# Kernel tuning notes

Hardware: AMD Instinct MI355X
Metric: run time of the kernel (lower is better)

## Reference

```python
import jax, jax.numpy as jnp
import numpy as np

B, S, H, U = 32, 2048, 1024, 1024


def setup_inputs() -> dict:
    key = jax.random.key(0)
    ks = jax.random.split(key, 5)
    sc = 1.0 / np.sqrt(H)
    return {
        "hidden_t": jax.random.normal(ks[0], (B, H), jnp.float32),
        "hiddens": jax.random.normal(ks[1], (B, S, H), jnp.float32),
        "W1": jax.random.normal(ks[2], (H, U), jnp.float32) * sc,
        "b1": jnp.zeros((U,), jnp.float32),
        "W2": jax.random.normal(ks[3], (H, U), jnp.float32) * sc,
        "b2": jnp.zeros((U,), jnp.float32),
        "V": jax.random.normal(ks[4], (U, 1), jnp.float32) * sc,
        "bV": jnp.zeros((1,), jnp.float32),
    }


def reference(hidden_t, hiddens, W1, b1, W2, b2, V, bV):
    # proj of encoder states: [B,S,U]; proj of decoder state broadcast over time: [B,1,U]
    keys = jnp.einsum("bsh,hu->bsu", hiddens, W1) + b1
    query = (hidden_t @ W2 + b2)[:, None, :]
    score = jnp.tanh(keys + query) @ V + bV            # [B,S,1]
    attention_weights = jax.nn.softmax(score, axis=1)  # softmax over seq axis
    context_vector = jnp.sum(attention_weights * hiddens, axis=1)  # [B,H]
    return context_vector, attention_weights
```

## Files before the change

### kernel.cpp

```cpp
#include <hip/hip_runtime.h>
#include <hip/hip_bf16.h>
#include <cstdint>

#define S_LEN 2048
#define B_SZ  32
#define H_DIM 1024
#define U_DIM 1024

#define BM 128
#define BN 128
#define BK 64

using short8  = __attribute__((ext_vector_type(8))) short;
using floatx4 = __attribute__((ext_vector_type(4))) float;

typedef __attribute__((address_space(3))) void lds_void;
typedef const __attribute__((address_space(1))) void glb_void;
#define GLD16(g, s) __builtin_amdgcn_global_load_lds((glb_void*)(g), (lds_void*)(s), 16, 0, 0)

__device__ __forceinline__ unsigned short f32_to_bf16_rne(float f) {
    unsigned int u = __float_as_uint(f);
    unsigned int r = (u + 0x7fffu + ((u >> 16) & 1u)) >> 16;
    return (unsigned short)r;
}

__global__ __launch_bounds__(256)
void cast_hiddens_kernel(const float* __restrict__ src, unsigned short* __restrict__ dst) {
    const size_t i = ((size_t)blockIdx.x * 256 + threadIdx.x) * 8;
    float4 a = *(const float4*)(src + i);
    float4 b = *(const float4*)(src + i + 4);
    ushort4 lo, hi;
    lo.x = f32_to_bf16_rne(a.x); lo.y = f32_to_bf16_rne(a.y);
    lo.z = f32_to_bf16_rne(a.z); lo.w = f32_to_bf16_rne(a.w);
    hi.x = f32_to_bf16_rne(b.x); hi.y = f32_to_bf16_rne(b.y);
    hi.z = f32_to_bf16_rne(b.z); hi.w = f32_to_bf16_rne(b.w);
    *(ushort4*)(dst + i)     = lo;
    *(ushort4*)(dst + i + 4) = hi;
}

__global__ void transpose_cast_w1(const float* __restrict__ W1,
                                  unsigned short* __restrict__ W1t) {
    __shared__ float tile[32][33];
    const int tx = threadIdx.x, ty = threadIdx.y;
    const int u0 = blockIdx.x * 32, h0 = blockIdx.y * 32;
#pragma unroll
    for (int i = 0; i < 4; ++i)
        tile[ty * 4 + i][tx] = W1[(size_t)(h0 + ty * 4 + i) * U_DIM + u0 + tx];
    __syncthreads();
#pragma unroll
    for (int i = 0; i < 4; ++i)
        W1t[(size_t)(u0 + ty * 4 + i) * H_DIM + h0 + tx] =
            f32_to_bf16_rne(tile[tx][ty * 4 + i]);
}

__global__ void query_kernel(const float* __restrict__ hidden_t,
                             const float* __restrict__ W2,
                             const float* __restrict__ b1,
                             const float* __restrict__ b2,
                             float* __restrict__ query) {
    const int b = blockIdx.y;
    const int u = blockIdx.x * 128 + threadIdx.x;
    const float* ht = hidden_t + b * H_DIM;
    float acc = b1[u] + b2[u];
#pragma unroll 8
    for (int h = 0; h < H_DIM; ++h)
        acc = fmaf(ht[h], W2[(size_t)h * U_DIM + u], acc);
    query[b * U_DIM + u] = acc;
}

__device__ __forceinline__ void score_epilogue(const floatx4 acc[4][4],
                                               const float* __restrict__ qrow,
                                               const float* __restrict__ V,
                                               float* __restrict__ scores,
                                               int m0, int n0, int wr, int wc, int q, int r) {
#pragma unroll
    for (int mt = 0; mt < 4; ++mt) {
#pragma unroll
        for (int reg = 0; reg < 4; ++reg) {
            float sum = 0.f;
#pragma unroll
            for (int nt = 0; nt < 4; ++nt) {
                const int c = n0 + wc * 64 + nt * 16 + r;
                float x = acc[mt][nt][reg] + qrow[c];
                x = fminf(fmaxf(x, -15.f), 15.f);
                float e = __expf(2.f * x);
                float t = (e - 1.f) / (e + 1.f);
                sum = fmaf(t, V[c], sum);
            }
            sum += __shfl_xor(sum, 1);
            sum += __shfl_xor(sum, 2);
            sum += __shfl_xor(sum, 4);
            sum += __shfl_xor(sum, 8);
            if (r == 0)
                atomicAdd(&scores[m0 + wr * 64 + mt * 16 + q * 4 + reg], sum);
        }
    }
}

__global__ __launch_bounds__(256)
void keys_score_v3(const unsigned short* __restrict__ hb,
                   const unsigned short* __restrict__ W1t,
                   const float* __restrict__ query,
                   const float* __restrict__ V,
                   float* __restrict__ scores) {
    __shared__ unsigned short As[BM * BK];
    __shared__ unsigned short Bs[BN * BK];

    const int tid = threadIdx.x;
    const int w = tid >> 6, l = tid & 63;
    const int q = l >> 4, r = l & 15;
    const int wr = w >> 1, wc = w & 1;

    const int bid = blockIdx.x;
    const int col      = (bid >> 3) & 7;
    const int row_band = ((bid >> 6) << 3) | (bid & 7);
    const int m0 = row_band * BM;
    const int n0 = col * BN;

    const int srow   = l >> 3;
    const int schunk = (l & 7) * 8;

    const unsigned short* gA = hb  + ((size_t)(m0 + w * 8 + srow) << 10) + schunk;
    const unsigned short* gB = W1t + ((size_t)(n0 + w * 8 + srow) << 10) + schunk;
    unsigned short* lA = &As[(w * 8) * BK];
    unsigned short* lB = &Bs[(w * 8) * BK];

    floatx4 acc[4][4];
#pragma unroll
    for (int mt = 0; mt < 4; ++mt)
#pragma unroll
        for (int nt = 0; nt < 4; ++nt)
            acc[mt][nt] = (floatx4){0.f, 0.f, 0.f, 0.f};

    for (int kt = 0; kt < H_DIM / BK; ++kt) {
#pragma unroll
        for (int i = 0; i < 4; ++i) {
            GLD16(gA + ((size_t)(i * 32) << 10), lA + i * 32 * BK);
            GLD16(gB + ((size_t)(i * 32) << 10), lB + i * 32 * BK);
        }
        gA += BK; gB += BK;

        __syncthreads();

#pragma unroll
        for (int kh = 0; kh < 2; ++kh) {
            short8 af[4], bfr[4];
#pragma unroll
            for (int mt = 0; mt < 4; ++mt)
                af[mt] = *(const short8*)&As[(wr * 64 + mt * 16 + r) * BK + kh * 32 + q * 8];
#pragma unroll
            for (int nt = 0; nt < 4; ++nt)
                bfr[nt] = *(const short8*)&Bs[(wc * 64 + nt * 16 + r) * BK + kh * 32 + q * 8];
#pragma unroll
            for (int mt = 0; mt < 4; ++mt)
#pragma unroll
                for (int nt = 0; nt < 4; ++nt)
                    acc[mt][nt] = __builtin_amdgcn_mfma_f32_16x16x32_bf16(
                        af[mt], bfr[nt], acc[mt][nt], 0, 0, 0);
        }

        __syncthreads();
    }

    const float* qrow = query + (m0 >> 11) * U_DIM;
    score_epilogue(acc, qrow, V, scores, m0, n0, wr, wc, q, r);
}

__global__ __launch_bounds__(256)
void keys_score_v1(const float* __restrict__ hiddens,
                   const unsigned short* __restrict__ W1t,
                   const float* __restrict__ query,
                   const float* __restrict__ V,
                   float* __restrict__ scores) {
    __shared__ unsigned short As[BM][40];
    __shared__ unsigned short Bs[BN][40];
    const int tid = threadIdx.x;
    const int lane = tid & 63, wave = tid >> 6;
    const int q = lane >> 4, r = lane & 15;
    const int wr = wave >> 1, wc = wave & 1;
    const int m0 = blockIdx.y * BM, n0 = blockIdx.x * BN;
    const int arow = tid >> 3, achunk = tid & 7;
    const int brow = tid >> 2, bchunk = tid & 3;
    floatx4 acc[4][4];
#pragma unroll
    for (int mt = 0; mt < 4; ++mt)
#pragma unroll
        for (int nt = 0; nt < 4; ++nt)
            acc[mt][nt] = (floatx4){0.f, 0.f, 0.f, 0.f};
    for (int kt = 0; kt < H_DIM / 32; ++kt) {
        const float* ag = hiddens + (size_t)(m0 + arow) * H_DIM + kt * 32 + achunk * 4;
#pragma unroll
        for (int i = 0; i < 4; ++i) {
            float4 f = *(const float4*)(ag + (size_t)i * 32 * H_DIM);
            ushort4 h;
            h.x = f32_to_bf16_rne(f.x); h.y = f32_to_bf16_rne(f.y);
            h.z = f32_to_bf16_rne(f.z); h.w = f32_to_bf16_rne(f.w);
            *(ushort4*)&As[arow + i * 32][achunk * 4] = h;
        }
        const unsigned short* bg = W1t + (size_t)(n0 + brow) * H_DIM + kt * 32 + bchunk * 8;
#pragma unroll
        for (int i = 0; i < 2; ++i)
            *(uint4*)&Bs[brow + i * 64][bchunk * 8] = *(const uint4*)(bg + (size_t)i * 64 * H_DIM);
        __syncthreads();
        short8 af[4], bfr[4];
#pragma unroll
        for (int mt = 0; mt < 4; ++mt)
            af[mt] = *(const short8*)&As[wr * 64 + mt * 16 + r][q * 8];
#pragma unroll
        for (int nt = 0; nt < 4; ++nt)
            bfr[nt] = *(const short8*)&Bs[wc * 64 + nt * 16 + r][q * 8];
#pragma unroll
        for (int mt = 0; mt < 4; ++mt)
#pragma unroll
            for (int nt = 0; nt < 4; ++nt)
                acc[mt][nt] = __builtin_amdgcn_mfma_f32_16x16x32_bf16(
                    af[mt], bfr[nt], acc[mt][nt], 0, 0, 0);
        __syncthreads();
    }
    const float* qrow = query + (m0 >> 11) * U_DIM;
    score_epilogue(acc, qrow, V, scores, m0, n0, wr, wc, q, r);
}

__global__ void softmax_kernel(const float* __restrict__ scores,
                               float* __restrict__ wout) {
    const int b = blockIdx.x, tid = threadIdx.x;
    const int wave = tid >> 6, lane = tid & 63;
    const float* src = scores + b * S_LEN;
    float v[8];
    float m = -1e30f;
#pragma unroll
    for (int i = 0; i < 8; ++i) { v[i] = src[tid + i * 256]; m = fmaxf(m, v[i]); }
#pragma unroll
    for (int off = 32; off >= 1; off >>= 1) m = fmaxf(m, __shfl_xor(m, off));
    __shared__ float red[4];
    if (lane == 0) red[wave] = m;
    __syncthreads();
    m = fmaxf(fmaxf(red[0], red[1]), fmaxf(red[2], red[3]));
    __syncthreads();
    float s = 0.f;
#pragma unroll
    for (int i = 0; i < 8; ++i) { v[i] = __expf(v[i] - m); s += v[i]; }
#pragma unroll
    for (int off = 32; off >= 1; off >>= 1) s += __shfl_xor(s, off);
    if (lane == 0) red[wave] = s;
    __syncthreads();
    s = red[0] + red[1] + red[2] + red[3];
    const float inv = 1.f / s;
#pragma unroll
    for (int i = 0; i < 8; ++i) wout[b * S_LEN + tid + i * 256] = v[i] * inv;
}

__global__ __launch_bounds__(256)
void context_kernel(const float* __restrict__ weights,
                    const float* __restrict__ hiddens,
                    float* __restrict__ out_ctx) {
    const int b = blockIdx.y;
    const int sc = blockIdx.x;
    const int h4 = threadIdx.x * 4;
    const float* wrow = weights + b * S_LEN + sc * 64;
    const float* hbase = hiddens + ((size_t)b * S_LEN + sc * 64) * H_DIM + h4;
    float4 acc = make_float4(0.f, 0.f, 0.f, 0.f);
    for (int s = 0; s < 64; ++s) {
        const float w = wrow[s];
        float4 hv = *(const float4*)(hbase + (size_t)s * H_DIM);
        acc.x = fmaf(w, hv.x, acc.x);
        acc.y = fmaf(w, hv.y, acc.y);
        acc.z = fmaf(w, hv.z, acc.z);
        acc.w = fmaf(w, hv.w, acc.w);
    }
    float* o = out_ctx + b * H_DIM + h4;
    atomicAdd(o + 0, acc.x);
    atomicAdd(o + 1, acc.y);
    atomicAdd(o + 2, acc.z);
    atomicAdd(o + 3, acc.w);
}

extern "C" void kernel_launch(void* const* d_in, const int* in_sizes, int n_in,
                              void* d_out, int out_size, void* d_ws, size_t ws_size,
                              hipStream_t stream) {
    const float* hidden_t = (const float*)d_in[0];
    const float* hiddens  = (const float*)d_in[1];
    const float* W1       = (const float*)d_in[2];
    const float* b1       = (const float*)d_in[3];
    const float* W2       = (const float*)d_in[4];
    const float* b2       = (const float*)d_in[5];
    const float* V        = (const float*)d_in[6];

    float* out_ctx = (float*)d_out;
    float* out_w   = (float*)d_out + B_SZ * H_DIM;

    char* ws = (char*)d_ws;
    unsigned short* W1t = (unsigned short*)ws;
    float* query  = (float*)(ws + (2u << 20));
    float* scores = query + B_SZ * U_DIM;
    unsigned short* hb = (unsigned short*)(ws + (4u << 20));
    const size_t need = (4u << 20) + (size_t)B_SZ * S_LEN * H_DIM * 2;

    hipMemsetAsync(scores, 0, (size_t)B_SZ * S_LEN * sizeof(float), stream);
    hipMemsetAsync(out_ctx, 0, (size_t)B_SZ * H_DIM * sizeof(float), stream);

    transpose_cast_w1<<<dim3(32, 32), dim3(32, 8), 0, stream>>>(W1, W1t);
    query_kernel<<<dim3(8, B_SZ), 128, 0, stream>>>(hidden_t, W2, b1, b2, query);

    if (ws_size >= need) {
        cast_hiddens_kernel<<<32768, 256, 0, stream>>>(hiddens, hb);
        keys_score_v3<<<(U_DIM / BN) * ((B_SZ * S_LEN) / BM), 256, 0, stream>>>(
            hb, W1t, query, V, scores);
    } else {
        keys_score_v1<<<dim3(U_DIM / 128, (B_SZ * S_LEN) / BM), 256, 0, stream>>>(
            hiddens, W1t, query, V, scores);
    }

    softmax_kernel<<<B_SZ, 256, 0, stream>>>(scores, out_w);
    context_kernel<<<dim3(S_LEN / 64, B_SZ), 256, 0, stream>>>(out_w, hiddens, out_ctx);
}
```

Before: 746.0 us.

## Swizzle GEMM LDS layout, split-K query projection, and finer context tiling

The bf16 GEMM's LDS tiles now use an XOR swizzle on the 16-byte chunk index for both the global-to-LDS writes and the MFMA fragment reads, to reduce LDS bank conflicts. The query projection is split along H into 8 chunks, each reduced with atomics into a zeroed buffer, to raise parallelism over the previous 256-block launch. The context kernel processes 32 sequence positions per block instead of 64, doubling the grid, and unrolls its loop. In exchange, the query and context outputs take more atomic traffic, and the query buffer needs an extra memset.

```diff
diff --git a/kernel.cpp b/kernel.cpp
--- a/kernel.cpp
+++ b/kernel.cpp
@@ -53,19 +53,22 @@
             f32_to_bf16_rne(tile[tx][ty * 4 + i]);
 }
 
-__global__ void query_kernel(const float* __restrict__ hidden_t,
-                             const float* __restrict__ W2,
-                             const float* __restrict__ b1,
-                             const float* __restrict__ b2,
-                             float* __restrict__ query) {
-    const int b = blockIdx.y;
-    const int u = blockIdx.x * 128 + threadIdx.x;
-    const float* ht = hidden_t + b * H_DIM;
-    float acc = b1[u] + b2[u];
+__global__ __launch_bounds__(128)
+void query_kernel_v2(const float* __restrict__ hidden_t,
+                     const float* __restrict__ W2,
+                     const float* __restrict__ b1,
+                     const float* __restrict__ b2,
+                     float* __restrict__ query) {
+    const int b  = blockIdx.z;
+    const int hc = blockIdx.y;
+    const int u  = blockIdx.x * 128 + threadIdx.x;
+    const float* ht = hidden_t + b * H_DIM + hc * 128;
+    const float* w  = W2 + (size_t)hc * 128 * U_DIM + u;
+    float acc = (hc == 0) ? (b1[u] + b2[u]) : 0.f;
 #pragma unroll 8
-    for (int h = 0; h < H_DIM; ++h)
-        acc = fmaf(ht[h], W2[(size_t)h * U_DIM + u], acc);
-    query[b * U_DIM + u] = acc;
+    for (int h = 0; h < 128; ++h)
+        acc = fmaf(ht[h], w[(size_t)h * U_DIM], acc);
+    atomicAdd(&query[b * U_DIM + u], acc);
 }
 
 __device__ __forceinline__ void score_epilogue(const floatx4 acc[4][4],
@@ -98,7 +101,7 @@
 }
 
 __global__ __launch_bounds__(256)
-void keys_score_v3(const unsigned short* __restrict__ hb,
+void keys_score_v4(const unsigned short* __restrict__ hb,
                    const unsigned short* __restrict__ W1t,
                    const float* __restrict__ query,
                    const float* __restrict__ V,
@@ -118,10 +121,10 @@
     const int n0 = col * BN;
 
     const int srow   = l >> 3;
-    const int schunk = (l & 7) * 8;
-
-    const unsigned short* gA = hb  + ((size_t)(m0 + w * 8 + srow) << 10) + schunk;
-    const unsigned short* gB = W1t + ((size_t)(n0 + w * 8 + srow) << 10) + schunk;
+    const int gchunk = ((l & 7) ^ srow) * 8;
+
+    const unsigned short* gA = hb  + ((size_t)(m0 + w * 8 + srow) << 10) + gchunk;
+    const unsigned short* gB = W1t + ((size_t)(n0 + w * 8 + srow) << 10) + gchunk;
     unsigned short* lA = &As[(w * 8) * BK];
     unsigned short* lB = &Bs[(w * 8) * BK];
 
@@ -132,6 +135,7 @@
         for (int nt = 0; nt < 4; ++nt)
             acc[mt][nt] = (floatx4){0.f, 0.f, 0.f, 0.f};
 
+    const int r7 = r & 7;
     for (int kt = 0; kt < H_DIM / BK; ++kt) {
 #pragma unroll
         for (int i = 0; i < 4; ++i) {
@@ -147,10 +151,12 @@
             short8 af[4], bfr[4];
 #pragma unroll
             for (int mt = 0; mt < 4; ++mt)
-                af[mt] = *(const short8*)&As[(wr * 64 + mt * 16 + r) * BK + kh * 32 + q * 8];
+                af[mt] = *(const short8*)
+                    &As[(wr * 64 + mt * 16 + r) * BK + (((kh << 2) | q) ^ r7) * 8];
 #pragma unroll
             for (int nt = 0; nt < 4; ++nt)
-                bfr[nt] = *(const short8*)&Bs[(wc * 64 + nt * 16 + r) * BK + kh * 32 + q * 8];
+                bfr[nt] = *(const short8*)
+                    &Bs[(wc * 64 + nt * 16 + r) * BK + (((kh << 2) | q) ^ r7) * 8];
 #pragma unroll
             for (int mt = 0; mt < 4; ++mt)
 #pragma unroll
@@ -257,10 +263,11 @@
     const int b = blockIdx.y;
     const int sc = blockIdx.x;
     const int h4 = threadIdx.x * 4;
-    const float* wrow = weights + b * S_LEN + sc * 64;
-    const float* hbase = hiddens + ((size_t)b * S_LEN + sc * 64) * H_DIM + h4;
+    const float* wrow = weights + b * S_LEN + sc * 32;
+    const float* hbase = hiddens + ((size_t)b * S_LEN + sc * 32) * H_DIM + h4;
     float4 acc = make_float4(0.f, 0.f, 0.f, 0.f);
-    for (int s = 0; s < 64; ++s) {
+#pragma unroll 4
+    for (int s = 0; s < 32; ++s) {
         const float w = wrow[s];
         float4 hv = *(const float4*)(hbase + (size_t)s * H_DIM);
         acc.x = fmaf(w, hv.x, acc.x);
@@ -296,15 +303,16 @@
     unsigned short* hb = (unsigned short*)(ws + (4u << 20));
     const size_t need = (4u << 20) + (size_t)B_SZ * S_LEN * H_DIM * 2;
 
+    hipMemsetAsync(query,  0, (size_t)B_SZ * U_DIM * sizeof(float), stream);
     hipMemsetAsync(scores, 0, (size_t)B_SZ * S_LEN * sizeof(float), stream);
     hipMemsetAsync(out_ctx, 0, (size_t)B_SZ * H_DIM * sizeof(float), stream);
 
     transpose_cast_w1<<<dim3(32, 32), dim3(32, 8), 0, stream>>>(W1, W1t);
-    query_kernel<<<dim3(8, B_SZ), 128, 0, stream>>>(hidden_t, W2, b1, b2, query);
+    query_kernel_v2<<<dim3(8, 8, B_SZ), 128, 0, stream>>>(hidden_t, W2, b1, b2, query);
 
     if (ws_size >= need) {
         cast_hiddens_kernel<<<32768, 256, 0, stream>>>(hiddens, hb);
-        keys_score_v3<<<(U_DIM / BN) * ((B_SZ * S_LEN) / BM), 256, 0, stream>>>(
+        keys_score_v4<<<(U_DIM / BN) * ((B_SZ * S_LEN) / BM), 256, 0, stream>>>(
             hb, W1t, query, V, scores);
     } else {
         keys_score_v1<<<dim3(U_DIM / 128, (B_SZ * S_LEN) / BM), 256, 0, stream>>>(
@@ -312,5 +320,5 @@
     }
 
     softmax_kernel<<<B_SZ, 256, 0, stream>>>(scores, out_w);
-    context_kernel<<<dim3(S_LEN / 64, B_SZ), 256, 0, stream>>>(out_w, hiddens, out_ctx);
-}
+    context_kernel<<<dim3(S_LEN / 32, B_SZ), 256, 0, stream>>>(out_w, hiddens, out_ctx);
+}
```

New measurement: 660.7 us. -11.4%, faster.
